# Optimization experiments

Measured on AMD Instinct MI355X. Metric: run time of the kernel, lower is better.

The kernel has to match this reference:

```python
import jax, jax.numpy as jnp
import numpy as np

B, S, E, H = 8, 3072, 512, 8  # batch, total seq (3 chunks of 1024), emb_size, num_heads


def setup_inputs() -> dict:
    key = jax.random.key(0)
    ks = jax.random.split(key, 9)
    sc = 0.02  # weight init scale
    return {
        "x": jax.random.normal(ks[0], (B, S, E), jnp.float32),
        "Wq": jax.random.normal(ks[1], (3, E, E), jnp.float32) * sc,
        "bq": jax.random.normal(ks[2], (3, E), jnp.float32) * sc,
        "Wk": jax.random.normal(ks[3], (3, E, E), jnp.float32) * sc,
        "bk": jax.random.normal(ks[4], (3, E), jnp.float32) * sc,
        "Wv": jax.random.normal(ks[5], (3, E, E), jnp.float32) * sc,
        "bv": jax.random.normal(ks[6], (3, E), jnp.float32) * sc,
        "Wp": jax.random.normal(ks[7], (3, E, E), jnp.float32) * sc,
        "bp": jax.random.normal(ks[8], (3, E), jnp.float32) * sc,
    }


def reference(x, Wq, bq, Wk, bk, Wv, bv, Wp, bp):
    b, s, e = x.shape
    d = e // H
    # split into 3 chunks along seq: xc[c] is chunk c, shape [b, n, e]
    xc = jnp.stack(jnp.split(x, 3, axis=1))  # [3, b, n, e]

    def lin(W, bias):  # torch Linear: x @ W.T + b, per chunk
        return jnp.einsum('cbne,cfe->cbnf', xc, W) + bias[:, None, None, :]

    def heads(t):  # [3, b, n, e] -> [3, b, h, n, d]
        c, bb, n, _ = t.shape
        return t.reshape(c, bb, n, H, d).transpose(0, 1, 3, 2, 4)

    q = heads(lin(Wq, bq))
    k = heads(lin(Wk, bk))
    v = heads(lin(Wv, bv))

    # rotated cross-chunk pairing (faithful to source):
    # out1 = attn(q2, k3, v3); out2 = attn(q3, k1, v1); out3 = attn(q1, k2, v2)
    q_sel = q[jnp.array([1, 2, 0])]
    k_sel = k[jnp.array([2, 0, 1])]
    v_sel = v[jnp.array([2, 0, 1])]

    scaling = jnp.sqrt(jnp.float32(e))  # note: sqrt(emb_size), not sqrt(head_dim)
    energy = jnp.einsum('cbhqd,cbhkd->cbhqk', q_sel, k_sel) / scaling
    att = jax.nn.softmax(energy, axis=-1)  # dropout: eval-mode identity
    out = jnp.einsum('cbhqk,cbhkd->cbhqd', att, v_sel)
    out = out.transpose(0, 1, 3, 2, 4).reshape(3, b, s // 3, e)  # merge heads
    out = jnp.einsum('cbne,cfe->cbnf', out, Wp) + bp[:, None, None, :]
    return jnp.concatenate([out[0], out[1], out[2]], axis=1)  # [b, s, e]
```

## Files before the change

kernel.cpp:

```cpp
#include <hip/hip_runtime.h>
#include <hip/hip_bf16.h>


typedef __attribute__((ext_vector_type(8))) short short8v;
typedef __attribute__((ext_vector_type(4))) float float4v;
typedef __attribute__((ext_vector_type(4))) unsigned short ushort4v;
typedef __attribute__((ext_vector_type(4))) unsigned int uint4v;

#define CHUNKS 3
#define BATCH 8
#define SEQ 3072
#define EMB 512
#define NH 8
#define HD 64
#define NCK 1024
#define MTOT (BATCH*SEQ)
#define QKV_ELEMS (CHUNKS*BATCH*NH*NCK*HD)
#define WELEMS (CHUNKS*EMB*EMB)
#define SM_SCALE 0.044194173824159216f

__device__ __forceinline__ unsigned short f2b(float f) {
  union { float f; unsigned int i; } x; x.f = f;
  unsigned int r = x.i + 0x7FFFu + ((x.i >> 16) & 1u);
  return (unsigned short)(r >> 16);
}
__device__ __forceinline__ unsigned int pack2r(float a, float b) {
  union { float f; unsigned int u; } xa, xb; xa.f = a; xb.f = b;
  return __builtin_amdgcn_perm(xb.u + 0x8000u, xa.u + 0x8000u, 0x07060302u);
}
__device__ __forceinline__ void gld_lds16(const unsigned short* g, unsigned short* l) {
  __builtin_amdgcn_global_load_lds(
      (const __attribute__((address_space(1))) unsigned int*)g,
      (__attribute__((address_space(3))) unsigned int*)l, 16, 0, 0);
}
#define MFMA(a, b, c) __builtin_amdgcn_mfma_f32_16x16x32_bf16(a, b, c, 0, 0, 0)

__global__ __launch_bounds__(256) void conv_x(
    const float* __restrict__ src, unsigned short* __restrict__ dst)
{
  size_t i = ((size_t)blockIdx.x * 256 + threadIdx.x) * 8;
  float4 a = *(const float4*)&src[i];
  float4 b = *(const float4*)&src[i + 4];
  uint4v p;
  p[0] = pack2r(a.x, a.y); p[1] = pack2r(a.z, a.w);
  p[2] = pack2r(b.x, b.y); p[3] = pack2r(b.z, b.w);
  *(uint4v*)&dst[i] = p;
}

__global__ __launch_bounds__(256) void conv_w(
    const float* __restrict__ s0, const float* __restrict__ s1,
    const float* __restrict__ s2, const float* __restrict__ s3,
    unsigned short* __restrict__ dst)
{
  const int z = blockIdx.y;
  const float* s = (z == 0) ? s0 : (z == 1) ? s1 : (z == 2) ? s2 : s3;
  size_t i = ((size_t)blockIdx.x * 256 + threadIdx.x) * 8;
  float4 a = *(const float4*)&s[i];
  float4 b = *(const float4*)&s[i + 4];
  uint4v p;
  p[0] = pack2r(a.x, a.y); p[1] = pack2r(a.z, a.w);
  p[2] = pack2r(b.x, b.y); p[3] = pack2r(b.z, b.w);
  *(uint4v*)&dst[(size_t)z * WELEMS + i] = p;
}

__global__ __launch_bounds__(256) void qkv_gemm(
    const unsigned short* __restrict__ xb, const unsigned short* __restrict__ Wb,
    const float* __restrict__ bq, const float* __restrict__ bk,
    const float* __restrict__ bv,
    unsigned short* __restrict__ qt, unsigned short* __restrict__ kt,
    unsigned short* __restrict__ vt)
{
  const int tid = threadIdx.x;
  const int w = tid >> 6, l = tid & 63;
  const int ln = l & 15, qu = l >> 4;
  const int sr = l >> 3, kbl = l & 7;
  const int row0 = blockIdx.x * 128;
  const int col0 = blockIdx.y * 128;
  const int z = blockIdx.z;
  const int bglob = row0 / SEQ;
  const int c = (row0 % SEQ) / NCK;
  const int n0 = row0 % NCK;
  const unsigned short* W = Wb + (size_t)z * WELEMS + c * EMB * EMB;
  const float* bias = (z == 0 ? bq : (z == 1 ? bk : bv)) + c * EMB;
  const float oscale = (z == 0) ? SM_SCALE : 1.0f;

  __shared__ unsigned short As[128 * 64];
  __shared__ unsigned short Bs[128 * 64];

  const int xo = (w & 1) * 64, fo = (w >> 1) * 64;

  float4v acc[4][4];
#pragma unroll
  for (int i = 0; i < 4; ++i)
#pragma unroll
    for (int j = 0; j < 4; ++j) acc[i][j] = (float4v){0.f, 0.f, 0.f, 0.f};

  for (int k0 = 0; k0 < EMB; k0 += 64) {
    __syncthreads();
#pragma unroll
    for (int s = 0; s < 4; ++s) {
      int rbase = w * 32 + s * 8;
      int r = rbase + sr;
      int kb_g = kbl ^ sr;
      gld_lds16(&xb[(size_t)(row0 + r) * EMB + k0 + kb_g * 8], &As[rbase * 64]);
      gld_lds16(&W [(size_t)(col0 + r) * EMB + k0 + kb_g * 8], &Bs[rbase * 64]);
    }
    __syncthreads();
#pragma unroll
    for (int ks = 0; ks < 2; ++ks) {
      short8v xf[4], wf[4];
#pragma unroll
      for (int i = 0; i < 4; ++i) {
        int rx = xo + 16 * i + ln;
        xf[i] = *(const short8v*)&As[rx * 64 + (((ks * 4 + qu) ^ (rx & 7)) * 8)];
        int rw = fo + 16 * i + ln;
        wf[i] = *(const short8v*)&Bs[rw * 64 + (((ks * 4 + qu) ^ (rw & 7)) * 8)];
      }
      if (z <= 1) {
#pragma unroll
        for (int i = 0; i < 4; ++i)
#pragma unroll
          for (int j = 0; j < 4; ++j) acc[i][j] = MFMA(wf[j], xf[i], acc[i][j]);
      } else {
#pragma unroll
        for (int i = 0; i < 4; ++i)
#pragma unroll
          for (int j = 0; j < 4; ++j) acc[i][j] = MFMA(xf[i], wf[j], acc[i][j]);
      }
    }
  }

  if (z <= 1) {
    unsigned short* outp = (z == 0) ? qt : kt;
#pragma unroll
    for (int j = 0; j < 4; ++j) {
      int f0 = col0 + fo + 16 * j + 4 * qu;
      float4 b4 = *(const float4*)&bias[f0];
      int hh = f0 >> 6, dd0 = f0 & 63;
      size_t base = ((size_t)((c * 8 + bglob) * 8 + hh)) << 16;
#pragma unroll
      for (int i = 0; i < 4; ++i) {
        int n = n0 + xo + 16 * i + ln;
        ushort4v p;
#pragma unroll
        for (int r = 0; r < 4; ++r)
          p[r] = f2b((acc[i][j][r] + ((const float*)&b4)[r]) * oscale);
        *(ushort4v*)&outp[base + (size_t)n * 64 + dd0] = p;
      }
    }
  } else {
#pragma unroll
    for (int i = 0; i < 4; ++i) {
      int nn0 = n0 + xo + 16 * i + 4 * qu;
#pragma unroll
      for (int j = 0; j < 4; ++j) {
        int f = col0 + fo + 16 * j + ln;
        int hh = f >> 6, dd = f & 63;
        float bvv = bias[f];
        size_t base = ((size_t)((c * 8 + bglob) * 8 + hh)) << 16;
        ushort4v p;
#pragma unroll
        for (int r = 0; r < 4; ++r) p[r] = f2b(acc[i][j][r] + bvv);
        *(ushort4v*)&vt[base + (size_t)dd * 1024 + nn0] = p;
      }
    }
  }
}

__global__ __launch_bounds__(256) void attn_kernel(
    const unsigned short* __restrict__ qt,
    const unsigned short* __restrict__ kt,
    const unsigned short* __restrict__ vt,
    unsigned short* __restrict__ attnb)
{
  const int tid = threadIdx.x;
  const int w = tid >> 6, l = tid & 63;
  const int ln = l & 15, qu = l >> 4;
  const int sr = l >> 3, kbl = l & 7;
  const int bid = blockIdx.x;
  const int hd = bid % 192;
  const int q0 = (bid / 192) * 128;
  const int co = hd >> 6;
  const int b  = (hd >> 3) & 7;
  const int h  = hd & 7;
  const int cq = (co + 1) % 3, ckv = (co + 2) % 3;
  const unsigned short* Qg = qt + ((size_t)((cq  * 8 + b) * 8 + h) << 16);
  const unsigned short* Kg = kt + ((size_t)((ckv * 8 + b) * 8 + h) << 16);
  const unsigned short* Vg = vt + ((size_t)((ckv * 8 + b) * 8 + h) << 16);

  __shared__ unsigned short Ks[64 * 64];
  __shared__ unsigned short Vs[64 * 64];
  __shared__ unsigned short Ps[4][32 * 36];

  short8v qf[2][2];
#pragma unroll
  for (int nt = 0; nt < 2; ++nt)
#pragma unroll
    for (int ks = 0; ks < 2; ++ks)
      qf[nt][ks] = *(const short8v*)&Qg[(size_t)(q0 + w * 32 + nt * 16 + ln) * 64 + ks * 32 + qu * 8];

  short8v onesf;
#pragma unroll
  for (int i = 0; i < 8; ++i) onesf[i] = (short)0x3F80;

  float4v acc_o[4][2];
#pragma unroll
  for (int i = 0; i < 4; ++i)
#pragma unroll
    for (int j = 0; j < 2; ++j) acc_o[i][j] = (float4v){0.f, 0.f, 0.f, 0.f};
  float4v acc_l[2];
  acc_l[0] = (float4v){0.f, 0.f, 0.f, 0.f};
  acc_l[1] = (float4v){0.f, 0.f, 0.f, 0.f};

  for (int kt0 = 0; kt0 < NCK; kt0 += 64) {
    __syncthreads();
#pragma unroll
    for (int s = 0; s < 2; ++s) {
      int r = w * 16 + s * 8;
      gld_lds16(&Kg[(size_t)(kt0 + r + sr) * 64 + ((kbl ^ sr) * 8)], &Ks[r * 64]);
      gld_lds16(&Vg[(size_t)(r + sr) * 1024 + kt0 + ((kbl ^ sr) * 8)], &Vs[r * 64]);
    }
    __syncthreads();

    float4v sacc[4][2];
#pragma unroll
    for (int mt = 0; mt < 4; ++mt)
#pragma unroll
      for (int nt = 0; nt < 2; ++nt) sacc[mt][nt] = (float4v){0.f, 0.f, 0.f, 0.f};
#pragma unroll
    for (int ks = 0; ks < 2; ++ks) {
#pragma unroll
      for (int mt = 0; mt < 4; ++mt) {
        int key = 16 * mt + ln;
        short8v kf = *(const short8v*)&Ks[key * 64 + (((ks * 4 + qu) ^ (key & 7)) * 8)];
#pragma unroll
        for (int nt = 0; nt < 2; ++nt)
          sacc[mt][nt] = MFMA(kf, qf[nt][ks], sacc[mt][nt]);
      }
    }

#pragma unroll
    for (int ks2 = 0; ks2 < 2; ++ks2) {
#pragma unroll
      for (int mh = 0; mh < 2; ++mh) {
        int mt = 2 * ks2 + mh;
#pragma unroll
        for (int nt = 0; nt < 2; ++nt) {
          float e0 = __expf(sacc[mt][nt][0]);
          float e1 = __expf(sacc[mt][nt][1]);
          float e2 = __expf(sacc[mt][nt][2]);
          float e3 = __expf(sacc[mt][nt][3]);
          uint4v pp;
          unsigned int u0 = pack2r(e0, e1), u1 = pack2r(e2, e3);
          *(unsigned int*)&Ps[w][(nt * 16 + ln) * 36 + 16 * mh + 4 * qu] = u0;
          *(unsigned int*)&Ps[w][(nt * 16 + ln) * 36 + 16 * mh + 4 * qu + 2] = u1;
          (void)pp;
        }
      }
      short8v pf[2], vf[4];
#pragma unroll
      for (int nt = 0; nt < 2; ++nt)
        pf[nt] = *(const short8v*)&Ps[w][(nt * 16 + ln) * 36 + qu * 8];
#pragma unroll
      for (int mt2 = 0; mt2 < 4; ++mt2) {
        int dd = 16 * mt2 + ln;
        vf[mt2] = *(const short8v*)&Vs[dd * 64 + (((ks2 * 4 + qu) ^ (dd & 7)) * 8)];
      }
#pragma unroll
      for (int nt = 0; nt < 2; ++nt)
        acc_l[nt] = MFMA(onesf, pf[nt], acc_l[nt]);
#pragma unroll
      for (int mt2 = 0; mt2 < 4; ++mt2)
#pragma unroll
        for (int nt = 0; nt < 2; ++nt)
          acc_o[mt2][nt] = MFMA(vf[mt2], pf[nt], acc_o[mt2][nt]);
    }
  }

  float inv[2];
  inv[0] = 1.0f / acc_l[0][0];
  inv[1] = 1.0f / acc_l[1][0];
  unsigned short* Og = attnb + (size_t)((co * 8 + b)) * NCK * EMB + h * HD;
#pragma unroll
  for (int mt = 0; mt < 4; ++mt) {
    int dd0 = 16 * mt + 4 * qu;
#pragma unroll
    for (int nt = 0; nt < 2; ++nt) {
      int q_glob = q0 + w * 32 + nt * 16 + ln;
      ushort4v p;
#pragma unroll
      for (int r = 0; r < 4; ++r) p[r] = f2b(acc_o[mt][nt][r] * inv[nt]);
      *(ushort4v*)&Og[(size_t)q_glob * EMB + dd0] = p;
    }
  }
}

__global__ __launch_bounds__(256) void proj_gemm(
    const unsigned short* __restrict__ attnb,
    const unsigned short* __restrict__ Wpb, const float* __restrict__ bp,
    float* __restrict__ out)
{
  const int tid = threadIdx.x;
  const int w = tid >> 6, l = tid & 63;
  const int ln = l & 15, qu = l >> 4;
  const int sr = l >> 3, kbl = l & 7;
  const int row0 = blockIdx.x * 128;
  const int col0 = blockIdx.y * 128;
  const int c = row0 >> 13;
  const int bglob = (row0 >> 10) & 7;
  const int n0 = row0 & 1023;
  const unsigned short* W = Wpb + c * EMB * EMB;
  const float* bias = bp + c * EMB;

  __shared__ unsigned short As[128 * 64];
  __shared__ unsigned short Bs[128 * 64];

  const int xo = (w & 1) * 64, fo = (w >> 1) * 64;

  float4v acc[4][4];
#pragma unroll
  for (int i = 0; i < 4; ++i)
#pragma unroll
    for (int j = 0; j < 4; ++j) acc[i][j] = (float4v){0.f, 0.f, 0.f, 0.f};

  for (int k0 = 0; k0 < EMB; k0 += 64) {
    __syncthreads();
#pragma unroll
    for (int s = 0; s < 4; ++s) {
      int rbase = w * 32 + s * 8;
      int r = rbase + sr;
      int kb_g = kbl ^ sr;
      gld_lds16(&attnb[(size_t)(row0 + r) * EMB + k0 + kb_g * 8], &As[rbase * 64]);
      gld_lds16(&W    [(size_t)(col0 + r) * EMB + k0 + kb_g * 8], &Bs[rbase * 64]);
    }
    __syncthreads();
#pragma unroll
    for (int ks = 0; ks < 2; ++ks) {
      short8v xf[4], wf[4];
#pragma unroll
      for (int i = 0; i < 4; ++i) {
        int rx = xo + 16 * i + ln;
        xf[i] = *(const short8v*)&As[rx * 64 + (((ks * 4 + qu) ^ (rx & 7)) * 8)];
        int rw = fo + 16 * i + ln;
        wf[i] = *(const short8v*)&Bs[rw * 64 + (((ks * 4 + qu) ^ (rw & 7)) * 8)];
      }
#pragma unroll
      for (int i = 0; i < 4; ++i)
#pragma unroll
        for (int j = 0; j < 4; ++j) acc[i][j] = MFMA(wf[j], xf[i], acc[i][j]);
    }
  }

#pragma unroll
  for (int j = 0; j < 4; ++j) {
    int f0 = col0 + fo + 16 * j + 4 * qu;
    float4 b4 = *(const float4*)&bias[f0];
#pragma unroll
    for (int i = 0; i < 4; ++i) {
      int srow = bglob * SEQ + c * NCK + n0 + xo + 16 * i + ln;
      float4 o;
      o.x = acc[i][j][0] + b4.x;
      o.y = acc[i][j][1] + b4.y;
      o.z = acc[i][j][2] + b4.z;
      o.w = acc[i][j][3] + b4.w;
      *(float4*)&out[(size_t)srow * EMB + f0] = o;
    }
  }
}

extern "C" void kernel_launch(void* const* d_in, const int* in_sizes, int n_in,
                              void* d_out, int out_size, void* d_ws, size_t ws_size,
                              hipStream_t stream) {
  (void)in_sizes; (void)n_in; (void)out_size; (void)ws_size;
  const float* x  = (const float*)d_in[0];
  const float* Wq = (const float*)d_in[1];
  const float* bq = (const float*)d_in[2];
  const float* Wk = (const float*)d_in[3];
  const float* bk = (const float*)d_in[4];
  const float* Wv = (const float*)d_in[5];
  const float* bv = (const float*)d_in[6];
  const float* Wp = (const float*)d_in[7];
  const float* bp = (const float*)d_in[8];
  float* out = (float*)d_out;

  unsigned short* Wb   = (unsigned short*)d_ws;
  unsigned short* qt   = Wb + 4 * (size_t)WELEMS;
  unsigned short* kt   = qt + QKV_ELEMS;
  unsigned short* vt   = kt + QKV_ELEMS;
  unsigned short* attn = vt + QKV_ELEMS;
  unsigned short* xbf  = attn;

  conv_x<<<QKV_ELEMS / (256 * 8), 256, 0, stream>>>(x, xbf);
  conv_w<<<dim3(WELEMS / (256 * 8), 4), 256, 0, stream>>>(Wq, Wk, Wv, Wp, Wb);
  qkv_gemm<<<dim3(MTOT / 128, EMB / 128, 3), 256, 0, stream>>>(
      xbf, Wb, bq, bk, bv, qt, kt, vt);
  attn_kernel<<<(NCK / 128) * CHUNKS * BATCH * NH, 256, 0, stream>>>(qt, kt, vt, attn);
  proj_gemm<<<dim3(MTOT / 128, EMB / 128), 256, 0, stream>>>(attn, Wb + 3 * (size_t)WELEMS, bp, out);
}
```

Measured before the change: 283.4 us.

## Double attention block to 512 threads, fold log2e into Q scale, use exp2

The attention kernel now runs 512 threads covering 256 queries per block, so each K/V tile loaded into LDS is shared by eight waves instead of four and each wave issues one load per tile. The Q scale absorbs log2(e) so the softmax can use the hardware exp2 instruction instead of __expf. P stores are merged into a single 8-byte write, and V fragment loads are interleaved with the MFMAs to lower register pressure. The grid shrinks to half as many blocks, which may reduce occupancy or load balance across CUs.

```diff
diff --git a/kernel.cpp b/kernel.cpp
--- a/kernel.cpp
+++ b/kernel.cpp
@@ -6,6 +6,7 @@
 typedef __attribute__((ext_vector_type(4))) float float4v;
 typedef __attribute__((ext_vector_type(4))) unsigned short ushort4v;
 typedef __attribute__((ext_vector_type(4))) unsigned int uint4v;
+typedef __attribute__((ext_vector_type(2))) unsigned int uint2v;
 
 #define CHUNKS 3
 #define BATCH 8
@@ -17,7 +18,7 @@
 #define MTOT (BATCH*SEQ)
 #define QKV_ELEMS (CHUNKS*BATCH*NH*NCK*HD)
 #define WELEMS (CHUNKS*EMB*EMB)
-#define SM_SCALE 0.044194173824159216f
+#define QSCALE 0.06375872465f
 
 __device__ __forceinline__ unsigned short f2b(float f) {
   union { float f; unsigned int i; } x; x.f = f;
@@ -82,7 +83,7 @@
   const int n0 = row0 % NCK;
   const unsigned short* W = Wb + (size_t)z * WELEMS + c * EMB * EMB;
   const float* bias = (z == 0 ? bq : (z == 1 ? bk : bv)) + c * EMB;
-  const float oscale = (z == 0) ? SM_SCALE : 1.0f;
+  const float oscale = (z == 0) ? QSCALE : 1.0f;
 
   __shared__ unsigned short As[128 * 64];
   __shared__ unsigned short Bs[128 * 64];
@@ -167,7 +168,7 @@
   }
 }
 
-__global__ __launch_bounds__(256) void attn_kernel(
+__global__ __launch_bounds__(512) void attn_kernel(
     const unsigned short* __restrict__ qt,
     const unsigned short* __restrict__ kt,
     const unsigned short* __restrict__ vt,
@@ -179,7 +180,7 @@
   const int sr = l >> 3, kbl = l & 7;
   const int bid = blockIdx.x;
   const int hd = bid % 192;
-  const int q0 = (bid / 192) * 128;
+  const int q0 = (bid / 192) * 256;
   const int co = hd >> 6;
   const int b  = (hd >> 3) & 7;
   const int h  = hd & 7;
@@ -190,7 +191,7 @@
 
   __shared__ unsigned short Ks[64 * 64];
   __shared__ unsigned short Vs[64 * 64];
-  __shared__ unsigned short Ps[4][32 * 36];
+  __shared__ unsigned short Ps[8][32 * 36];
 
   short8v qf[2][2];
 #pragma unroll
@@ -214,9 +215,8 @@
 
   for (int kt0 = 0; kt0 < NCK; kt0 += 64) {
     __syncthreads();
-#pragma unroll
-    for (int s = 0; s < 2; ++s) {
-      int r = w * 16 + s * 8;
+    {
+      int r = w * 8;
       gld_lds16(&Kg[(size_t)(kt0 + r + sr) * 64 + ((kbl ^ sr) * 8)], &Ks[r * 64]);
       gld_lds16(&Vg[(size_t)(r + sr) * 1024 + kt0 + ((kbl ^ sr) * 8)], &Vs[r * 64]);
     }
@@ -246,34 +246,31 @@
         int mt = 2 * ks2 + mh;
 #pragma unroll
         for (int nt = 0; nt < 2; ++nt) {
-          float e0 = __expf(sacc[mt][nt][0]);
-          float e1 = __expf(sacc[mt][nt][1]);
-          float e2 = __expf(sacc[mt][nt][2]);
-          float e3 = __expf(sacc[mt][nt][3]);
-          uint4v pp;
-          unsigned int u0 = pack2r(e0, e1), u1 = pack2r(e2, e3);
-          *(unsigned int*)&Ps[w][(nt * 16 + ln) * 36 + 16 * mh + 4 * qu] = u0;
-          *(unsigned int*)&Ps[w][(nt * 16 + ln) * 36 + 16 * mh + 4 * qu + 2] = u1;
-          (void)pp;
+          float e0 = __builtin_amdgcn_exp2f(sacc[mt][nt][0]);
+          float e1 = __builtin_amdgcn_exp2f(sacc[mt][nt][1]);
+          float e2 = __builtin_amdgcn_exp2f(sacc[mt][nt][2]);
+          float e3 = __builtin_amdgcn_exp2f(sacc[mt][nt][3]);
+          uint2v u;
+          u[0] = pack2r(e0, e1);
+          u[1] = pack2r(e2, e3);
+          *(uint2v*)&Ps[w][(nt * 16 + ln) * 36 + 16 * mh + 4 * qu] = u;
         }
       }
-      short8v pf[2], vf[4];
+      short8v pf[2];
 #pragma unroll
       for (int nt = 0; nt < 2; ++nt)
         pf[nt] = *(const short8v*)&Ps[w][(nt * 16 + ln) * 36 + qu * 8];
 #pragma unroll
+      for (int nt = 0; nt < 2; ++nt)
+        acc_l[nt] = MFMA(onesf, pf[nt], acc_l[nt]);
+#pragma unroll
       for (int mt2 = 0; mt2 < 4; ++mt2) {
         int dd = 16 * mt2 + ln;
-        vf[mt2] = *(const short8v*)&Vs[dd * 64 + (((ks2 * 4 + qu) ^ (dd & 7)) * 8)];
-      }
-#pragma unroll
-      for (int nt = 0; nt < 2; ++nt)
-        acc_l[nt] = MFMA(onesf, pf[nt], acc_l[nt]);
-#pragma unroll
-      for (int mt2 = 0; mt2 < 4; ++mt2)
+        short8v vf = *(const short8v*)&Vs[dd * 64 + (((ks2 * 4 + qu) ^ (dd & 7)) * 8)];
 #pragma unroll
         for (int nt = 0; nt < 2; ++nt)
-          acc_o[mt2][nt] = MFMA(vf[mt2], pf[nt], acc_o[mt2][nt]);
+          acc_o[mt2][nt] = MFMA(vf, pf[nt], acc_o[mt2][nt]);
+      }
     }
   }
 
@@ -394,6 +391,6 @@
   conv_w<<<dim3(WELEMS / (256 * 8), 4), 256, 0, stream>>>(Wq, Wk, Wv, Wp, Wb);
   qkv_gemm<<<dim3(MTOT / 128, EMB / 128, 3), 256, 0, stream>>>(
       xbf, Wb, bq, bk, bv, qt, kt, vt);
-  attn_kernel<<<(NCK / 128) * CHUNKS * BATCH * NH, 256, 0, stream>>>(qt, kt, vt, attn);
+  attn_kernel<<<(NCK / 256) * CHUNKS * BATCH * NH, 512, 0, stream>>>(qt, kt, vt, attn);
   proj_gemm<<<dim3(MTOT / 128, EMB / 128), 256, 0, stream>>>(attn, Wb + 3 * (size_t)WELEMS, bp, out);
 }
```

Result: faster. 265.5 us (-6.3%).
